# Kernel optimization log

Hardware: AMD Instinct MI355X
Metric: run time of the kernel (lower is better)

The kernel has to match this reference:

```python
import jax, jax.numpy as jnp
import numpy as np

T, N, E = 6, 10000, 50000
D_IN, D, HEADS, W = 64, 64, 4, 8
TAUS = (4.0, 16.0)
N_FREQ = 3
D_PE = len(TAUS) + 2 * N_FREQ  # 8
TEMP = 1.0
EPS_GATE = 1e-6
NEG_INF = -1e30


def _rel_encoding():
    # RelativeTimeEncoding: multi-scale exp decays + sin/cos features over dt in [0, W];
    # rel_bias is a monotone recency bias -log(1+dt).
    dt = jnp.arange(W + 1, dtype=jnp.float32)
    decays = jnp.exp(-dt[:, None] / jnp.asarray(TAUS, dtype=jnp.float32))  # (W+1, 2)
    freqs = 1.0 / (2.0 ** jnp.arange(N_FREQ, dtype=jnp.float32))  # (3,)
    ang = dt[:, None] * freqs  # (W+1, 3)
    pe = jnp.concatenate([decays, jnp.sin(ang), jnp.cos(ang)], axis=-1)  # (W+1, D_PE)
    bias = -jnp.log1p(dt)  # (W+1,)
    return pe, bias


def setup_inputs() -> dict:
    key = jax.random.key(0)
    ks = jax.random.split(key, 6)
    H_tilde = jax.random.normal(ks[0], (T, N, D_IN), dtype=jnp.float32)
    S = jax.random.uniform(ks[1], (T, N), dtype=jnp.float32)  # spike gates in [0,1)
    edge_index = jax.random.randint(ks[2], (2, E), 0, N)
    time_idx = jnp.arange(T)
    # xavier_uniform like torch Linear weights [out, in]
    lim_q = (6.0 / (D_IN + D)) ** 0.5
    W_q = jax.random.uniform(ks[3], (D, D_IN), jnp.float32, -lim_q, lim_q)
    lim_k = (6.0 / (D_IN + D_PE + D)) ** 0.5
    W_k = jax.random.uniform(ks[4], (D, D_IN + D_PE), jnp.float32, -lim_k, lim_k)
    W_v = jax.random.uniform(ks[5], (D, D_IN), jnp.float32, -lim_q, lim_q)
    return {"H_tilde": H_tilde, "S": S, "W_q": W_q, "W_k": W_k, "W_v": W_v,
            "edge_index": edge_index, "time_idx": time_idx}


def _forward(H_tilde, S, W_q, W_k, W_v, edge_index):
    heads, dh = HEADS, D // HEADS
    scale = dh ** -0.5
    src, dst = edge_index[0], edge_index[1]
    pe_table, rel_bias = _rel_encoding()
    Q_all = (H_tilde @ W_q.T).reshape(T, N, heads, dh)  # (T, N, h, dh)
    dt = jnp.arange(W + 1)
    seg = jnp.tile(dst, W + 1)              # ((W+1)*E,) segment ids
    pe_w = jnp.broadcast_to(pe_table[:, None, :], (W + 1, E, D_PE))

    def step(carry, t):
        valid = dt <= t                      # (W+1,) mask replaces the W_eff=min(W,t) truncation
        tp = jnp.clip(t - dt, 0)             # (W+1,) source timesteps
        Qd = Q_all[t][dst]                   # (E, h, dh)
        Hs = H_tilde[tp][:, src, :]          # (W+1, E, d_in) windowed gather
        Kw = (jnp.concatenate([Hs, pe_w], axis=-1) @ W_k.T).reshape(W + 1, E, heads, dh)
        Vw = (Hs @ W_v.T).reshape(W + 1, E, heads, dh)
        gate = jnp.log(S[tp][:, src] + EPS_GATE)  # (W+1, E) log-gating
        scores = jnp.einsum('ehd,wehd->weh', Qd, Kw) * scale  # (W+1, E, h)
        scores = (scores + rel_bias[:, None, None] + gate[..., None]) / TEMP
        scores = jnp.where(valid[:, None, None], scores, NEG_INF)
        sflat = scores.reshape(-1, heads)    # ((W+1)*E, h)
        smax = jax.ops.segment_max(sflat, seg, num_segments=N)  # (N, h) segment amax
        vflat = jnp.repeat(valid, E)
        ex = jnp.exp(sflat - smax[seg]) * vflat[:, None].astype(sflat.dtype)
        Vflat = Vw.reshape(-1, heads, dh)
        numer = jax.ops.segment_sum(ex[..., None] * Vflat, seg, num_segments=N)  # (N, h, dh)
        denom = jax.ops.segment_sum(ex, seg, num_segments=N)                     # (N, h)
        msg = numer / jnp.clip(denom, 1e-12)[..., None]
        return carry, msg.reshape(N, D)

    _, M_out = jax.lax.scan(step, None, jnp.arange(T))
    return M_out  # (T, N, d)


def reference(H_tilde, S, W_q, W_k, W_v, edge_index, time_idx):
    return _forward(H_tilde, S, W_q, W_k, W_v, edge_index)
```

## Files before the change

### kernel.cpp

```cpp
#include <hip/hip_runtime.h>
#include <hip/hip_bf16.h>

#define T_DIM 6
#define N_NODES 10000
#define TOTAL_ROWS (T_DIM * N_NODES)
#define LOG2E 1.44269504088896340736f
#define QPRE (0.25f * LOG2E)
#define EPS_GATE 1e-6f
#define NEGBIG (-1e30f)
#define CAP 64
#define REC 832

typedef unsigned int u32;
typedef unsigned short u16;
typedef __attribute__((ext_vector_type(8))) short bf16x8;
typedef __attribute__((ext_vector_type(4))) float f32x4;

#define MFMA16(a, b, c) __builtin_amdgcn_mfma_f32_16x16x32_bf16(a, b, c, 0, 0, 0)

__device__ __forceinline__ float fast_exp2(float x) {
#if __has_builtin(__builtin_amdgcn_exp2f)
    return __builtin_amdgcn_exp2f(x);
#else
    return exp2f(x);
#endif
}

template <int CTRL>
__device__ __forceinline__ float dpp_add(float x) {
    int v = __builtin_amdgcn_update_dpp(0, __float_as_int(x), CTRL, 0xf, 0xf, true);
    return x + __int_as_float(v);
}
__device__ __forceinline__ float red4(float x) {
    x = dpp_add<0xB1>(x);
    x = dpp_add<0x4E>(x);
    return x;
}

__device__ __forceinline__ float bf2f(u16 u) {
    union { unsigned int i; float f; } c;
    c.i = ((unsigned int)u) << 16;
    return c.f;
}

__device__ __forceinline__ u16 f2bf(float f) {
    union { float f; unsigned int i; } c; c.f = f;
    unsigned int i = c.i;
    unsigned int lsb = (i >> 16) & 1u;
    i += 0x7FFFu + lsb;
    return (u16)(i >> 16);
}

__global__ __launch_bounds__(256) void proj_kernel(
    const float* __restrict__ H,
    const float* __restrict__ S,
    const float* __restrict__ Wq, const float* __restrict__ Wk,
    const float* __restrict__ Wv,
    int* __restrict__ cursor,
    float* __restrict__ Qs, u16* __restrict__ KVG,
    float* __restrict__ kpe, float* __restrict__ bias) {
    int tid = threadIdx.x;
    int gtid = blockIdx.x * 256 + tid;
    if (gtid < N_NODES) {
        cursor[gtid] = 0;
        float* gp = (float*)(KVG + (size_t)gtid * REC + 768);
        #pragma unroll
        for (int t = 0; t < T_DIM; ++t)
            gp[t] = log2f(S[t * N_NODES + gtid] + EPS_GATE);
    }
    if (blockIdx.x == 0 && tid < 64) {
        int c = tid;
        for (int dt = 0; dt < 9; ++dt) {
            float fdt = (float)dt;
            float pe[8];
            pe[0] = expf(-fdt * 0.25f);
            pe[1] = expf(-fdt * 0.0625f);
            pe[2] = sinf(fdt * 1.0f);
            pe[3] = sinf(fdt * 0.5f);
            pe[4] = sinf(fdt * 0.25f);
            pe[5] = cosf(fdt * 1.0f);
            pe[6] = cosf(fdt * 0.5f);
            pe[7] = cosf(fdt * 0.25f);
            float acc = 0.f;
            #pragma unroll
            for (int j = 0; j < 8; ++j) acc += pe[j] * Wk[c * 72 + 64 + j];
            kpe[dt * 64 + c] = acc;
            if (c == 0) bias[dt] = -log2f(1.0f + fdt);
        }
    }

    __shared__ short whi[192][72];
    __shared__ short wlo[192][72];
    for (int i = tid; i < 192 * 64; i += 256) {
        int col = i >> 6, k = i & 63;
        float w;
        if (col < 64)       w = Wq[col * 64 + k];
        else if (col < 128) w = Wk[(col - 64) * 72 + k];
        else                w = Wv[(col - 128) * 64 + k];
        u16 hb = f2bf(w);
        whi[col][k] = (short)hb;
        wlo[col][k] = (short)f2bf(w - bf2f(hb));
    }
    __syncthreads();

    int lane = tid & 63, wid = tid >> 6;
    int r0 = (blockIdx.x * 4 + wid) * 32;
    if (r0 >= TOTAL_ROWS) return;

    int mrow = lane & 15;
    int kgrp = lane >> 4;

    bf16x8 ahi[2][2], alo[2][2];
    #pragma unroll
    for (int mt = 0; mt < 2; ++mt) {
        #pragma unroll
        for (int ks = 0; ks < 2; ++ks) {
            const float* hp = H + (size_t)(r0 + mt * 16 + mrow) * 64 + ks * 32 + kgrp * 8;
            float4 hA = *(const float4*)hp;
            float4 hB = *(const float4*)(hp + 4);
            float tmp[8] = {hA.x, hA.y, hA.z, hA.w, hB.x, hB.y, hB.z, hB.w};
            #pragma unroll
            for (int b = 0; b < 8; ++b) {
                u16 hb = f2bf(tmp[b]);
                ahi[mt][ks][b] = (short)hb;
                alo[mt][ks][b] = (short)f2bf(tmp[b] - bf2f(hb));
            }
        }
    }

    #pragma unroll
    for (int nt = 0; nt < 12; ++nt) {
        f32x4 acc0 = {0.f, 0.f, 0.f, 0.f};
        f32x4 acc1 = {0.f, 0.f, 0.f, 0.f};
        #pragma unroll
        for (int ks = 0; ks < 2; ++ks) {
            bf16x8 bh = *(const bf16x8*)&whi[nt * 16 + mrow][ks * 32 + kgrp * 8];
            bf16x8 bl = *(const bf16x8*)&wlo[nt * 16 + mrow][ks * 32 + kgrp * 8];
            acc0 = MFMA16(ahi[0][ks], bh, acc0);
            acc0 = MFMA16(ahi[0][ks], bl, acc0);
            acc0 = MFMA16(alo[0][ks], bh, acc0);
            acc1 = MFMA16(ahi[1][ks], bh, acc1);
            acc1 = MFMA16(ahi[1][ks], bl, acc1);
            acc1 = MFMA16(alo[1][ks], bh, acc1);
        }
        #pragma unroll
        for (int mt = 0; mt < 2; ++mt) {
            f32x4 acc = mt ? acc1 : acc0;
            int mbase = r0 + mt * 16 + kgrp * 4;
            #pragma unroll
            for (int j = 0; j < 4; ++j) {
                int gr = mbase + j;
                float v = acc[j];
                int t = gr / N_NODES, n = gr - t * N_NODES;
                int col = (nt & 3) * 16 + mrow;
                if (nt < 4)      Qs[(size_t)gr * 64 + col] = v * QPRE;
                else if (nt < 8) KVG[(size_t)n * REC + t * 64 + col] = f2bf(v);
                else             KVG[(size_t)n * REC + 384 + t * 64 + col] = f2bf(v);
            }
        }
    }
}

__global__ void scatter_kernel(const int* __restrict__ esrc, const int* __restrict__ edst,
                               int* __restrict__ cursor, int* __restrict__ slots, int E) {
    int e = blockIdx.x * blockDim.x + threadIdx.x;
    if (e < E) {
        int d = edst[e];
        int pos = atomicAdd(&cursor[d], 1);
        if (pos < CAP) slots[d * CAP + pos] = esrc[e];
    }
}

__global__ __launch_bounds__(256) void agg_kernel(
    const float* __restrict__ Qs,
    const u16* __restrict__ KVG,
    const float* __restrict__ kpe,
    const float* __restrict__ bias,
    const int* __restrict__ deg_arr,
    const int* __restrict__ slots,
    float* __restrict__ out) {
    int lane = threadIdx.x & 63, w = threadIdx.x >> 6;
    int n = blockIdx.x * 4 + w;
    int e4 = lane >> 4;
    int doff = (lane & 15) << 2;

    int deg = deg_arr[n];
    if (deg <= 0) {
        if (e4 == 0) {
            #pragma unroll
            for (int t = 0; t < T_DIM; ++t)
                *(float4*)(out + ((size_t)t * N_NODES + n) * 64 + doff) =
                    make_float4(0.f, 0.f, 0.f, 0.f);
        }
        return;
    }
    deg = min(deg, CAP);
    int slotv = slots[n * CAP + lane];

    float4 q[T_DIM];
    #pragma unroll
    for (int t = 0; t < T_DIM; ++t)
        q[t] = *(const float4*)(Qs + ((size_t)t * N_NODES + n) * 64 + doff);

    float cc[21];
    #pragma unroll
    for (int dt = 0; dt < T_DIM; ++dt) {
        float4 kp = *(const float4*)(kpe + dt * 64 + doff);
        float b = bias[dt];
        #pragma unroll
        for (int t = dt; t < T_DIM; ++t) {
            float part = q[t].x * kp.x;
            part = fmaf(q[t].y, kp.y, part);
            part = fmaf(q[t].z, kp.z, part);
            part = fmaf(q[t].w, kp.w, part);
            cc[t * (t + 1) / 2 + dt] = red4(part) + b;
        }
    }

    float den[T_DIM] = {0,0,0,0,0,0};
    float4 nu[T_DIM];
    #pragma unroll
    for (int t = 0; t < T_DIM; ++t) nu[t] = make_float4(0.f, 0.f, 0.f, 0.f);

    int ng = (deg + 3) >> 2;
    uint2 ku[T_DIM], vu[T_DIM];
    float gg[T_DIM];

    {
        int eidx = e4;
        int s = __shfl(slotv, min(eidx, deg - 1));
        const u16* base = KVG + (size_t)s * REC;
        #pragma unroll
        for (int t = 0; t < T_DIM; ++t) {
            ku[t] = *(const uint2*)(base + t * 64 + doff);
            vu[t] = *(const uint2*)(base + 384 + t * 64 + doff);
        }
        const float* gp = (const float*)(base + 768);
        bool val = eidx < deg;
        #pragma unroll
        for (int t = 0; t < T_DIM; ++t) gg[t] = val ? gp[t] : NEGBIG;
    }

    for (int g = 0; g < ng; ++g) {
        uint2 ku2[T_DIM], vu2[T_DIM];
        float gg2[T_DIM];
        {
            int eidx = (g + 1) * 4 + e4;
            int s = __shfl(slotv, min(eidx, deg - 1));
            const u16* base = KVG + (size_t)s * REC;
            #pragma unroll
            for (int t = 0; t < T_DIM; ++t) {
                ku2[t] = *(const uint2*)(base + t * 64 + doff);
                vu2[t] = *(const uint2*)(base + 384 + t * 64 + doff);
            }
            const float* gp = (const float*)(base + 768);
            bool val = eidx < deg;
            #pragma unroll
            for (int t = 0; t < T_DIM; ++t) gg2[t] = val ? gp[t] : NEGBIG;
        }
        #pragma unroll
        for (int tp = 0; tp < T_DIM; ++tp) {
            float k0 = bf2f((u16)(ku[tp].x & 0xffff));
            float k1 = bf2f((u16)(ku[tp].x >> 16));
            float k2 = bf2f((u16)(ku[tp].y & 0xffff));
            float k3 = bf2f((u16)(ku[tp].y >> 16));
            float v0 = bf2f((u16)(vu[tp].x & 0xffff));
            float v1 = bf2f((u16)(vu[tp].x >> 16));
            float v2 = bf2f((u16)(vu[tp].y & 0xffff));
            float v3 = bf2f((u16)(vu[tp].y >> 16));
            float gv = gg[tp];
            #pragma unroll
            for (int t = tp; t < T_DIM; ++t) {
                int dt = t - tp;
                float part = q[t].x * k0;
                part = fmaf(q[t].y, k1, part);
                part = fmaf(q[t].z, k2, part);
                part = fmaf(q[t].w, k3, part);
                float wt = fast_exp2(red4(part) + cc[t * (t + 1) / 2 + dt] + gv);
                den[t] += wt;
                nu[t].x = fmaf(wt, v0, nu[t].x);
                nu[t].y = fmaf(wt, v1, nu[t].y);
                nu[t].z = fmaf(wt, v2, nu[t].z);
                nu[t].w = fmaf(wt, v3, nu[t].w);
            }
        }
        #pragma unroll
        for (int t = 0; t < T_DIM; ++t) { ku[t] = ku2[t]; vu[t] = vu2[t]; gg[t] = gg2[t]; }
    }

    #pragma unroll
    for (int t = 0; t < T_DIM; ++t) {
        den[t] += __shfl_xor(den[t], 16);  den[t] += __shfl_xor(den[t], 32);
        nu[t].x += __shfl_xor(nu[t].x, 16); nu[t].x += __shfl_xor(nu[t].x, 32);
        nu[t].y += __shfl_xor(nu[t].y, 16); nu[t].y += __shfl_xor(nu[t].y, 32);
        nu[t].z += __shfl_xor(nu[t].z, 16); nu[t].z += __shfl_xor(nu[t].z, 32);
        nu[t].w += __shfl_xor(nu[t].w, 16); nu[t].w += __shfl_xor(nu[t].w, 32);
    }
    if (e4 == 0) {
        #pragma unroll
        for (int t = 0; t < T_DIM; ++t) {
            float r = 1.0f / fmaxf(den[t], 1e-12f);
            *(float4*)(out + ((size_t)t * N_NODES + n) * 64 + doff) =
                make_float4(nu[t].x * r, nu[t].y * r, nu[t].z * r, nu[t].w * r);
        }
    }
}

extern "C" void kernel_launch(void* const* d_in, const int* in_sizes, int n_in,
                              void* d_out, int out_size, void* d_ws, size_t ws_size,
                              hipStream_t stream) {
    const float* H  = (const float*)d_in[0];
    const float* S  = (const float*)d_in[1];
    const float* Wq = (const float*)d_in[2];
    const float* Wk = (const float*)d_in[3];
    const float* Wv = (const float*)d_in[4];
    const int* edge = (const int*)d_in[5];
    int E = in_sizes[5] / 2;
    const int* esrc = edge;
    const int* edst = edge + E;
    float* out = (float*)d_out;

    char* ws = (char*)d_ws;
    size_t off = 0;
    auto alloc = [&](size_t b) { char* p = ws + off; off += (b + 255) & ~(size_t)255; return (void*)p; };
    u16*   KVG     = (u16*)  alloc((size_t)N_NODES * REC * 2);
    int*   cursor  = (int*)  alloc((size_t)N_NODES * 4);
    int*   slots   = (int*)  alloc((size_t)N_NODES * CAP * 4);
    float* kpe     = (float*)alloc(9 * 64 * 4);
    float* bias    = (float*)alloc(9 * 4);

    int proj_blocks = (TOTAL_ROWS / 32 + 3) / 4;
    proj_kernel<<<proj_blocks, 256, 0, stream>>>(H, S, Wq, Wk, Wv, cursor, out, KVG, kpe, bias);
    scatter_kernel<<<(E + 255) / 256, 256, 0, stream>>>(esrc, edst, cursor, slots, E);
    agg_kernel<<<(N_NODES + 3) / 4, 256, 0, stream>>>(out, KVG, kpe, bias, cursor, slots, out);
}
```

Before: 57.82 us.

## Interleave K/V in bf16 records, store Q as bf16, deepen gather prefetch

K and V are now stored interleaved per timestep, so each lane fetches one 16-byte load per timestep instead of two 8-byte loads. Q is written as bf16 to a separate workspace buffer rather than fp32 into the output buffer, and it is loaded early, before the degree check. The gather loop now prefetches two edge groups ahead, and blocks shrink to 128 threads (2 nodes each). The aim is fewer, wider memory transactions and more latency hiding, at the cost of extra Q precision loss and possibly more register pressure.

```diff
diff --git a/kernel.cpp b/kernel.cpp
--- a/kernel.cpp
+++ b/kernel.cpp
@@ -57,7 +57,7 @@
     const float* __restrict__ Wq, const float* __restrict__ Wk,
     const float* __restrict__ Wv,
     int* __restrict__ cursor,
-    float* __restrict__ Qs, u16* __restrict__ KVG,
+    u16* __restrict__ Qb, u16* __restrict__ KVG,
     float* __restrict__ kpe, float* __restrict__ bias) {
     int tid = threadIdx.x;
     int gtid = blockIdx.x * 256 + tid;
@@ -153,9 +153,9 @@
                 float v = acc[j];
                 int t = gr / N_NODES, n = gr - t * N_NODES;
                 int col = (nt & 3) * 16 + mrow;
-                if (nt < 4)      Qs[(size_t)gr * 64 + col] = v * QPRE;
-                else if (nt < 8) KVG[(size_t)n * REC + t * 64 + col] = f2bf(v);
-                else             KVG[(size_t)n * REC + 384 + t * 64 + col] = f2bf(v);
+                if (nt < 4)      Qb[(size_t)gr * 64 + col] = f2bf(v * QPRE);
+                else if (nt < 8) KVG[(size_t)n * REC + t * 128 + col * 2] = f2bf(v);
+                else             KVG[(size_t)n * REC + t * 128 + col * 2 + 1] = f2bf(v);
             }
         }
     }
@@ -171,8 +171,8 @@
     }
 }
 
-__global__ __launch_bounds__(256) void agg_kernel(
-    const float* __restrict__ Qs,
+__global__ __launch_bounds__(128) void agg_kernel(
+    const u16* __restrict__ Qb,
     const u16* __restrict__ KVG,
     const float* __restrict__ kpe,
     const float* __restrict__ bias,
@@ -180,11 +180,17 @@
     const int* __restrict__ slots,
     float* __restrict__ out) {
     int lane = threadIdx.x & 63, w = threadIdx.x >> 6;
-    int n = blockIdx.x * 4 + w;
+    int n = blockIdx.x * 2 + w;
     int e4 = lane >> 4;
     int doff = (lane & 15) << 2;
 
     int deg = deg_arr[n];
+    int slotv = slots[n * CAP + lane];
+    uint2 qraw[T_DIM];
+    #pragma unroll
+    for (int t = 0; t < T_DIM; ++t)
+        qraw[t] = *(const uint2*)(Qb + ((size_t)t * N_NODES + n) * 64 + doff);
+
     if (deg <= 0) {
         if (e4 == 0) {
             #pragma unroll
@@ -195,13 +201,38 @@
         return;
     }
     deg = min(deg, CAP);
-    int slotv = slots[n * CAP + lane];
+    int ng = (deg + 3) >> 2;
+
+    uint4 kvA[T_DIM], kvB[T_DIM];
+    float ggA[T_DIM], ggB[T_DIM];
+
+#define LOADG(BASE, KV, GG) {                                                   \
+        int eidx = (BASE) + e4;                                                 \
+        int sidx = __shfl(slotv, min(eidx, deg - 1));                           \
+        const u16* bp = KVG + (size_t)sidx * REC;                               \
+        _Pragma("unroll")                                                       \
+        for (int t = 0; t < T_DIM; ++t)                                         \
+            KV[t] = *(const uint4*)(bp + t * 128 + doff * 2);                   \
+        const float* gp = (const float*)(bp + 768);                             \
+        float4 gA = *(const float4*)gp;                                         \
+        float2 gB = *(const float2*)(gp + 4);                                   \
+        bool val = eidx < deg;                                                  \
+        GG[0] = val ? gA.x : NEGBIG; GG[1] = val ? gA.y : NEGBIG;               \
+        GG[2] = val ? gA.z : NEGBIG; GG[3] = val ? gA.w : NEGBIG;               \
+        GG[4] = val ? gB.x : NEGBIG; GG[5] = val ? gB.y : NEGBIG;               \
+    }
+
+    LOADG(0, kvA, ggA);
+    if (ng > 1) LOADG(4, kvB, ggB);
 
     float4 q[T_DIM];
     #pragma unroll
-    for (int t = 0; t < T_DIM; ++t)
-        q[t] = *(const float4*)(Qs + ((size_t)t * N_NODES + n) * 64 + doff);
-
+    for (int t = 0; t < T_DIM; ++t) {
+        q[t].x = bf2f((u16)(qraw[t].x & 0xffff));
+        q[t].y = bf2f((u16)(qraw[t].x >> 16));
+        q[t].z = bf2f((u16)(qraw[t].y & 0xffff));
+        q[t].w = bf2f((u16)(qraw[t].y >> 16));
+    }
     float cc[21];
     #pragma unroll
     for (int dt = 0; dt < T_DIM; ++dt) {
@@ -222,53 +253,15 @@
     #pragma unroll
     for (int t = 0; t < T_DIM; ++t) nu[t] = make_float4(0.f, 0.f, 0.f, 0.f);
 
-    int ng = (deg + 3) >> 2;
-    uint2 ku[T_DIM], vu[T_DIM];
-    float gg[T_DIM];
-
-    {
-        int eidx = e4;
-        int s = __shfl(slotv, min(eidx, deg - 1));
-        const u16* base = KVG + (size_t)s * REC;
-        #pragma unroll
-        for (int t = 0; t < T_DIM; ++t) {
-            ku[t] = *(const uint2*)(base + t * 64 + doff);
-            vu[t] = *(const uint2*)(base + 384 + t * 64 + doff);
-        }
-        const float* gp = (const float*)(base + 768);
-        bool val = eidx < deg;
-        #pragma unroll
-        for (int t = 0; t < T_DIM; ++t) gg[t] = val ? gp[t] : NEGBIG;
-    }
-
-    for (int g = 0; g < ng; ++g) {
-        uint2 ku2[T_DIM], vu2[T_DIM];
-        float gg2[T_DIM];
-        {
-            int eidx = (g + 1) * 4 + e4;
-            int s = __shfl(slotv, min(eidx, deg - 1));
-            const u16* base = KVG + (size_t)s * REC;
-            #pragma unroll
-            for (int t = 0; t < T_DIM; ++t) {
-                ku2[t] = *(const uint2*)(base + t * 64 + doff);
-                vu2[t] = *(const uint2*)(base + 384 + t * 64 + doff);
-            }
-            const float* gp = (const float*)(base + 768);
-            bool val = eidx < deg;
-            #pragma unroll
-            for (int t = 0; t < T_DIM; ++t) gg2[t] = val ? gp[t] : NEGBIG;
-        }
+    for (int g = 0; ; ++g) {
         #pragma unroll
         for (int tp = 0; tp < T_DIM; ++tp) {
-            float k0 = bf2f((u16)(ku[tp].x & 0xffff));
-            float k1 = bf2f((u16)(ku[tp].x >> 16));
-            float k2 = bf2f((u16)(ku[tp].y & 0xffff));
-            float k3 = bf2f((u16)(ku[tp].y >> 16));
-            float v0 = bf2f((u16)(vu[tp].x & 0xffff));
-            float v1 = bf2f((u16)(vu[tp].x >> 16));
-            float v2 = bf2f((u16)(vu[tp].y & 0xffff));
-            float v3 = bf2f((u16)(vu[tp].y >> 16));
-            float gv = gg[tp];
+            uint4 x = kvA[tp];
+            float k0 = bf2f((u16)(x.x & 0xffff)), v0 = bf2f((u16)(x.x >> 16));
+            float k1 = bf2f((u16)(x.y & 0xffff)), v1 = bf2f((u16)(x.y >> 16));
+            float k2 = bf2f((u16)(x.z & 0xffff)), v2 = bf2f((u16)(x.z >> 16));
+            float k3 = bf2f((u16)(x.w & 0xffff)), v3 = bf2f((u16)(x.w >> 16));
+            float gv = ggA[tp];
             #pragma unroll
             for (int t = tp; t < T_DIM; ++t) {
                 int dt = t - tp;
@@ -284,9 +277,12 @@
                 nu[t].w = fmaf(wt, v3, nu[t].w);
             }
         }
-        #pragma unroll
-        for (int t = 0; t < T_DIM; ++t) { ku[t] = ku2[t]; vu[t] = vu2[t]; gg[t] = gg2[t]; }
-    }
+        if (g + 1 >= ng) break;
+        #pragma unroll
+        for (int t = 0; t < T_DIM; ++t) { kvA[t] = kvB[t]; ggA[t] = ggB[t]; }
+        if (g + 2 < ng) LOADG((g + 2) * 4, kvB, ggB);
+    }
+#undef LOADG
 
     #pragma unroll
     for (int t = 0; t < T_DIM; ++t) {
@@ -324,13 +320,14 @@
     size_t off = 0;
     auto alloc = [&](size_t b) { char* p = ws + off; off += (b + 255) & ~(size_t)255; return (void*)p; };
     u16*   KVG     = (u16*)  alloc((size_t)N_NODES * REC * 2);
+    u16*   Qb      = (u16*)  alloc((size_t)TOTAL_ROWS * 64 * 2);
     int*   cursor  = (int*)  alloc((size_t)N_NODES * 4);
     int*   slots   = (int*)  alloc((size_t)N_NODES * CAP * 4);
     float* kpe     = (float*)alloc(9 * 64 * 4);
     float* bias    = (float*)alloc(9 * 4);
 
     int proj_blocks = (TOTAL_ROWS / 32 + 3) / 4;
-    proj_kernel<<<proj_blocks, 256, 0, stream>>>(H, S, Wq, Wk, Wv, cursor, out, KVG, kpe, bias);
+    proj_kernel<<<proj_blocks, 256, 0, stream>>>(H, S, Wq, Wk, Wv, cursor, Qb, KVG, kpe, bias);
     scatter_kernel<<<(E + 255) / 256, 256, 0, stream>>>(esrc, edst, cursor, slots, E);
-    agg_kernel<<<(N_NODES + 3) / 4, 256, 0, stream>>>(out, KVG, kpe, bias, cursor, slots, out);
-}
+    agg_kernel<<<(N_NODES + 1) / 2, 128, 0, stream>>>(Qb, KVG, kpe, bias, cursor, slots, out);
+}
```

Result: faster. 56.39 us (-2.5%).
